# Optimization experiments

Measured on AMD Instinct MI355X. Metric: run time of the kernel, lower is better.

The kernel has to match this reference:

```python
import jax, jax.numpy as jnp
import numpy as np

COMMITMENT_COST = 0.25
NUM_EMBEDDINGS = 1024
EMBEDDING_DIM = 64


def setup_inputs() -> dict:
    key = jax.random.key(0)
    k1, k2 = jax.random.split(key)
    x = jax.random.normal(k1, (32, 64, 64, 64), dtype=jnp.float32)
    embeddings = jax.random.normal(k2, (EMBEDDING_DIM, NUM_EMBEDDINGS), dtype=jnp.float32)
    return {"x": x, "embeddings": embeddings}


def reference(x, embeddings):
    # x: [..., D], embeddings: [D, K]
    flat = jnp.reshape(x, (-1, EMBEDDING_DIM))                       # [N, D]
    # squared euclidean distances via ||a||^2 - 2 a.e + ||e||^2      # [N, K]
    distances = (jnp.sum(flat * flat, axis=1, keepdims=True)
                 - 2.0 * (flat @ embeddings)
                 + jnp.sum(embeddings * embeddings, axis=0, keepdims=True))
    flat_indices = jnp.argmax(-distances, axis=1)                    # [N]
    encodings = jax.nn.one_hot(flat_indices, NUM_EMBEDDINGS, dtype=distances.dtype)  # [N, K]
    encoding_indices = jnp.reshape(flat_indices, x.shape[:-1])
    # gather codebook rows: embeddings.T[idx]
    quantized = jnp.take(embeddings.T, encoding_indices, axis=0)     # same shape as x
    e_latent_loss = jnp.mean((jax.lax.stop_gradient(quantized) - x) ** 2)
    q_latent_loss = jnp.mean((quantized - jax.lax.stop_gradient(x)) ** 2)
    loss = q_latent_loss + COMMITMENT_COST * e_latent_loss
    quantized_st = x + jax.lax.stop_gradient(quantized - x)          # straight-through
    avg_probs = jnp.mean(encodings, axis=0)                          # [K]
    perplexity = jnp.exp(-jnp.sum(avg_probs * jnp.log(avg_probs + 1e-10)))
    return quantized_st, loss, perplexity, encodings, encoding_indices, distances
```

## Files before the change

kernel.cpp:

```cpp
#include <hip/hip_runtime.h>
#include <hip/hip_bf16.h>
#include <math.h>

#define NROWS 131072
#define DDIM  64
#define KCODE 1024
#define TAU_B 0.008f

#define OFF_Q    0L
#define OFF_LOSS 8388608L
#define OFF_PERP 8388609L
#define OFF_ENC  8388610L
#define OFF_IDX  (OFF_ENC + 134217728L)
#define OFF_DIST (OFF_IDX + 131072L)

#define WS_ENORM 0L
#define WS_ET    1024L
#define WS_EBPH  66560L
#define WS_EBPL  99328L
#define WS_CNT   263168L
#define WS_PART  395268L

typedef short bf16x8 __attribute__((ext_vector_type(8)));
typedef float f32x4  __attribute__((ext_vector_type(4)));
typedef float f32x2  __attribute__((ext_vector_type(2)));
typedef _Float16 f16x4v __attribute__((ext_vector_type(4)));

__device__ inline unsigned short f2bf(float f) {
    unsigned u = __float_as_uint(f);
    unsigned r = (u + 0x7fffu + ((u >> 16) & 1u)) >> 16;
    return (unsigned short)r;
}
__device__ inline float bf2f(unsigned short h) {
    return __uint_as_float(((unsigned)h) << 16);
}
__device__ inline int dswz16(int i) { return i ^ (((i >> 12) & 3) << 3); }

__global__ __launch_bounds__(256) void k1a_prep(const float* __restrict__ e,
                                                float* __restrict__ enorm,
                                                float* __restrict__ eT,
                                                int* __restrict__ cnt) {
    int k = blockIdx.x * 256 + threadIdx.x;
    float s = 0.f;
    #pragma unroll 8
    for (int d = 0; d < DDIM; ++d) {
        float v = e[(size_t)d * KCODE + k];
        s = fmaf(v, v, s);
        eT[(size_t)k * DDIM + d] = v;
    }
    enorm[k] = s;
    cnt[k] = 0;
}

__global__ __launch_bounds__(128) void k1b_pack(const float* __restrict__ e,
                                                unsigned short* __restrict__ ebph,
                                                unsigned short* __restrict__ ebpl) {
    const int gct = blockIdx.x;
    const int ks  = threadIdx.x >> 6;
    const int l   = threadIdx.x & 63;
    const int col = (gct << 4) | (l & 15);
    const int kb  = (ks << 5) + ((l >> 4) << 3);
    const size_t ob = ((size_t)((gct << 1) | ks) * 64 + l) * 8;
    #pragma unroll
    for (int j = 0; j < 8; ++j) {
        float f = e[(size_t)(kb + j) * KCODE + col];
        unsigned short h = f2bf(f);
        float lo = f - bf2f(h);
        ebph[ob + j] = h;
        ebpl[ob + j] = f2bf(lo);
    }
}

__global__ __launch_bounds__(256, 4) void kA_fused(const float* __restrict__ x,
                                                   const float* __restrict__ e,
                                                   const unsigned short* __restrict__ ebph,
                                                   const unsigned short* __restrict__ ebpl,
                                                   const float* __restrict__ enorm,
                                                   const float* __restrict__ eT,
                                                   float* __restrict__ dist,
                                                   float* __restrict__ enc,
                                                   float* __restrict__ outq,
                                                   float* __restrict__ outidx,
                                                   int* __restrict__ cnt,
                                                   float* __restrict__ partials) {
    __shared__ __align__(16) _Float16 dtH[16384];
    __shared__ float hd[2];
    __shared__ short xh[16 * 64];
    __shared__ short xl[16 * 64];
    __shared__ float xn[16];
    __shared__ float wm1[4][16], wm2[4][16];
    __shared__ int   wi1[4][16];
    __shared__ float ps[16];
    __shared__ int   sidx[16];
    __shared__ int   nearmask;
    __shared__ float xsh[DDIM];
    __shared__ double wbv[4];
    __shared__ int    wbi[4];

    const int tid  = threadIdx.x;
    const int lane = tid & 63;
    const int w    = tid >> 6;
    const int rowbase = blockIdx.x * 16;
    float* ebase = enc + ((size_t)blockIdx.x << 14);

    {
        if (tid == 0) nearmask = 0;
        float4 v = ((const float4*)(x + (size_t)rowbase * DDIM))[tid];
        int fi = tid * 4, r = fi >> 6, c = fi & 63;
        float fv[4] = {v.x, v.y, v.z, v.w};
        short hv[4], lv[4];
        #pragma unroll
        for (int q = 0; q < 4; ++q) {
            unsigned short hh = f2bf(fv[q]);
            hv[q] = (short)hh;
            lv[q] = (short)f2bf(fv[q] - bf2f(hh));
        }
        *(short4*)&xh[r * 64 + c] = make_short4(hv[0], hv[1], hv[2], hv[3]);
        *(short4*)&xl[r * 64 + c] = make_short4(lv[0], lv[1], lv[2], lv[3]);
        float s4 = fmaf(v.x, v.x, fmaf(v.y, v.y, fmaf(v.z, v.z, v.w * v.w)));
        #pragma unroll
        for (int m = 1; m < 16; m <<= 1) s4 += __shfl_xor(s4, m);
        if ((lane & 15) == 0) xn[r] = s4;
    }
    __syncthreads();

    const int arow = lane & 15, akb = (lane >> 4) << 3;
    bf16x8 ah0 = *(const bf16x8*)&xh[arow * 64 + akb];
    bf16x8 ah1 = *(const bf16x8*)&xh[arow * 64 + 32 + akb];
    bf16x8 al0 = *(const bf16x8*)&xl[arow * 64 + akb];
    bf16x8 al1 = *(const bf16x8*)&xl[arow * 64 + 32 + akb];

    const int wr   = (lane >> 4) << 2;
    const int colb = (w << 8) | (lane & 15);
    float xnv[4];
    #pragma unroll
    for (int r = 0; r < 4; ++r) xnv[r] = xn[wr + r];
    float env[16];
    #pragma unroll
    for (int ct = 0; ct < 16; ++ct) env[ct] = enorm[colb + (ct << 4)];

    float m1[4], m2[4];
    int   i1[4];
    #pragma unroll
    for (int r = 0; r < 4; ++r) { m1[r] = 3.4e38f; m2[r] = 3.4e38f; i1[r] = 1 << 30; }

    const f32x4 z4 = {0.f, 0.f, 0.f, 0.f};

    #pragma unroll 4
    for (int ct = 0; ct < 16; ++ct) {
        const int gct = (w << 4) | ct;
        const size_t bo = ((size_t)(gct << 1) * 64 + lane) * 8;
        bf16x8 bh0 = *(const bf16x8*)(ebph + bo);
        bf16x8 bh1 = *(const bf16x8*)(ebph + bo + 512);
        bf16x8 bl0 = *(const bf16x8*)(ebpl + bo);
        bf16x8 bl1 = *(const bf16x8*)(ebpl + bo + 512);

        {
            const int s = (ct << 8) + tid;
            if (s < 4095) {
                *(f32x4*)(ebase + 2 + (s << 2)) = z4;
            } else {
                *(f32x2*)(ebase)         = (f32x2){0.f, 0.f};
                *(f32x2*)(ebase + 16382) = (f32x2){0.f, 0.f};
            }
        }

        f32x4 d = {0.f, 0.f, 0.f, 0.f};
        d = __builtin_amdgcn_mfma_f32_16x16x32_bf16(ah0, bh0, d, 0, 0, 0);
        d = __builtin_amdgcn_mfma_f32_16x16x32_bf16(ah1, bh1, d, 0, 0, 0);
        d = __builtin_amdgcn_mfma_f32_16x16x32_bf16(ah0, bl0, d, 0, 0, 0);
        d = __builtin_amdgcn_mfma_f32_16x16x32_bf16(ah1, bl1, d, 0, 0, 0);
        d = __builtin_amdgcn_mfma_f32_16x16x32_bf16(al0, bh0, d, 0, 0, 0);
        d = __builtin_amdgcn_mfma_f32_16x16x32_bf16(al1, bh1, d, 0, 0, 0);

        const int col = colb + (ct << 4);
        #pragma unroll
        for (int r = 0; r < 4; ++r) {
            float o = fmaf(-2.f, d[r], xnv[r] + env[ct]);
            if (o < m1[r]) { m2[r] = m1[r]; m1[r] = o; i1[r] = col; }
            else if (o < m2[r]) m2[r] = o;
            const int fl = ((wr + r) << 10) + col;
            if (fl >= 2) dtH[dswz16(fl - 2)] = (_Float16)o;
            else         hd[fl] = o;
        }
    }

    #pragma unroll
    for (int m = 1; m < 16; m <<= 1) {
        #pragma unroll
        for (int r = 0; r < 4; ++r) {
            float om1 = __shfl_xor(m1[r], m);
            int   oi1 = __shfl_xor(i1[r], m);
            float om2 = __shfl_xor(m2[r], m);
            if (om1 < m1[r] || (om1 == m1[r] && oi1 < i1[r])) {
                m2[r] = fminf(m1[r], om2); m1[r] = om1; i1[r] = oi1;
            } else {
                m2[r] = fminf(m2[r], om1);
            }
        }
    }
    if ((lane & 15) == 0) {
        #pragma unroll
        for (int r = 0; r < 4; ++r) {
            wm1[w][wr + r] = m1[r];
            wm2[w][wr + r] = m2[r];
            wi1[w][wr + r] = i1[r];
        }
    }
    __syncthreads();
    if (tid < 16) {
        float bm1 = wm1[0][tid], bm2 = wm2[0][tid];
        int   bi  = wi1[0][tid];
        #pragma unroll
        for (int wv = 1; wv < 4; ++wv) {
            float om1 = wm1[wv][tid], om2 = wm2[wv][tid];
            int   oi  = wi1[wv][tid];
            if (om1 < bm1 || (om1 == bm1 && oi < bi)) {
                bm2 = fminf(bm1, om2); bm1 = om1; bi = oi;
            } else {
                bm2 = fminf(bm2, om1);
            }
        }
        sidx[tid] = bi;
        ps[tid]   = bm1;
        if (bm2 - bm1 < TAU_B) atomicOr(&nearmask, 1 << tid);
    }
    __syncthreads();

    {
        float* dbase = dist + ((size_t)rowbase << 10);
        #pragma unroll
        for (int j = 0; j < 16; ++j) {
            const int s = (j << 8) + tid;
            if (s < 4095) {
                const int i0 = s << 2;
                const int iw = dswz16(i0);
                f16x4v h = *(const f16x4v*)&dtH[iw];
                f32x4 v = {(float)h[0], (float)h[1], (float)h[2], (float)h[3]};
                *(f32x4*)(dbase + 2 + i0) = v;
            }
        }
        if (tid == 255) {
            const int it = dswz16(16380);
            *(f32x2*)(dbase)         = (f32x2){hd[0], hd[1]};
            *(f32x2*)(dbase + 16382) = (f32x2){(float)dtH[it], (float)dtH[it + 1]};
        }
    }

    if (nearmask) {
        for (int mrow = nearmask; mrow; mrow &= (mrow - 1)) {
            const int r = __ffs(mrow) - 1;
            if (tid < DDIM) xsh[tid] = x[(size_t)(rowbase + r) * DDIM + tid];
            __syncthreads();
            const int k0 = tid * 4;
            double dd[4] = {0.0, 0.0, 0.0, 0.0};
            for (int d = 0; d < DDIM; ++d) {
                double xd = (double)xsh[d];
                float4 ev = *(const float4*)(e + (size_t)d * KCODE + k0);
                double t0 = xd - (double)ev.x; dd[0] = fma(t0, t0, dd[0]);
                double t1 = xd - (double)ev.y; dd[1] = fma(t1, t1, dd[1]);
                double t2 = xd - (double)ev.z; dd[2] = fma(t2, t2, dd[2]);
                double t3 = xd - (double)ev.w; dd[3] = fma(t3, t3, dd[3]);
            }
            double best = dd[0]; int bidx = k0;
            #pragma unroll
            for (int c = 1; c < 4; ++c)
                if (dd[c] < best) { best = dd[c]; bidx = k0 + c; }
            #pragma unroll
            for (int m = 1; m < 64; m <<= 1) {
                double ob = __shfl_xor(best, m);
                int    oi = __shfl_xor(bidx, m);
                if (ob < best || (ob == best && oi < bidx)) { best = ob; bidx = oi; }
            }
            if (lane == 0) { wbv[w] = best; wbi[w] = bidx; }
            __syncthreads();
            if (tid == 0) {
                double bb = wbv[0]; int bi = wbi[0];
                #pragma unroll
                for (int wv = 1; wv < 4; ++wv)
                    if (wbv[wv] < bb || (wbv[wv] == bb && wbi[wv] < bi)) {
                        bb = wbv[wv]; bi = wbi[wv];
                    }
                sidx[r] = bi; ps[r] = (float)bb;
            }
            __syncthreads();
        }
    }

    if (tid < 16) {
        const int idx = sidx[tid];
        ebase[((size_t)tid << 10) + idx] = 1.0f;
        outidx[rowbase + tid] = (float)idx;
        atomicAdd(cnt + idx, 1);
    }
    {
        const int r = tid >> 4, c = tid & 15;
        const int idx = sidx[r];
        f32x4 ev = *(const f32x4*)(eT + (size_t)idx * DDIM + (c << 2));
        *((f32x4*)(outq + ((size_t)(rowbase + r) << 6)) + c) = ev;
    }
    if (tid == 64) {
        float s = 0.f;
        #pragma unroll
        for (int j = 0; j < 16; ++j) s += ps[j];
        partials[blockIdx.x] = s;
    }
}

__global__ __launch_bounds__(256) void k6_scalar(const float* __restrict__ partials,
                                                 const int* __restrict__ cnt,
                                                 float* __restrict__ outloss,
                                                 float* __restrict__ outperp) {
    __shared__ double sd[256];
    const int tid = threadIdx.x;
    double s = 0.0;
    for (int i = tid; i < 8192; i += 256) s += (double)partials[i];
    sd[tid] = s;
    __syncthreads();
    for (int st = 128; st > 0; st >>= 1) {
        if (tid < st) sd[tid] += sd[tid + st];
        __syncthreads();
    }
    const double total = sd[0];
    __syncthreads();
    double h = 0.0;
    for (int k = tid; k < KCODE; k += 256) {
        double p = (double)cnt[k] / (double)NROWS;
        h -= p * log(p + 1e-10);
    }
    sd[tid] = h;
    __syncthreads();
    for (int st = 128; st > 0; st >>= 1) {
        if (tid < st) sd[tid] += sd[tid + st];
        __syncthreads();
    }
    if (tid == 0) {
        *outloss = (float)(total * 1.25 / (double)((long)NROWS * DDIM));
        *outperp = (float)exp(sd[0]);
    }
}

extern "C" void kernel_launch(void* const* d_in, const int* in_sizes, int n_in,
                              void* d_out, int out_size, void* d_ws, size_t ws_size,
                              hipStream_t stream) {
    const float* x = (const float*)d_in[0];
    const float* e = (const float*)d_in[1];
    float* out = (float*)d_out;

    float* ws_f = (float*)d_ws;
    float* enorm   = ws_f + WS_ENORM;
    float* eT      = ws_f + WS_ET;
    unsigned short* ebph = (unsigned short*)(ws_f + WS_EBPH);
    unsigned short* ebpl = (unsigned short*)(ws_f + WS_EBPL);
    int*   cnt     = (int*)(ws_f + WS_CNT);
    float* partials= ws_f + WS_PART;

    float* outq    = out + OFF_Q;
    float* outloss = out + OFF_LOSS;
    float* outperp = out + OFF_PERP;
    float* enc     = out + OFF_ENC;
    float* outidx  = out + OFF_IDX;
    float* dist    = out + OFF_DIST;

    hipLaunchKernelGGL(k1a_prep, dim3(4),    dim3(256), 0, stream, e, enorm, eT, cnt);
    hipLaunchKernelGGL(k1b_pack, dim3(64),   dim3(128), 0, stream, e, ebph, ebpl);
    hipLaunchKernelGGL(kA_fused, dim3(8192), dim3(256), 0, stream, x, e, ebph, ebpl, enorm,
                       eT, dist, enc, outq, outidx, cnt, partials);
    hipLaunchKernelGGL(k6_scalar,dim3(1),    dim3(256), 0, stream, partials, cnt, outloss, outperp);
}
```

Before: 283.3 us.

## Make each wave own 16 rows over all codes, removing block-level barriers

Each wave now processes 16 rows across the full 1024-code codebook instead of splitting columns across four waves, so the cross-wave min reduction and __syncthreads barriers go away. Distances are staged in per-wave LDS in four 256-column chunks and streamed out right after each chunk, and the fp64 near-tie refinement runs per wave with 16 codes per lane. The grid shrinks to 2048 blocks of 64 rows. In exchange, each wave now reads the whole packed codebook and does a longer serial loop. The dist stores are only 8-byte aligned because of an offset of 2 floats.

```diff
diff --git a/kernel.cpp b/kernel.cpp
--- a/kernel.cpp
+++ b/kernel.cpp
@@ -25,6 +25,7 @@
 typedef float f32x4  __attribute__((ext_vector_type(4)));
 typedef float f32x2  __attribute__((ext_vector_type(2)));
 typedef _Float16 f16x4v __attribute__((ext_vector_type(4)));
+typedef float f32x4u __attribute__((ext_vector_type(4), aligned(8)));
 
 __device__ inline unsigned short f2bf(float f) {
     unsigned u = __float_as_uint(f);
@@ -34,7 +35,7 @@
 __device__ inline float bf2f(unsigned short h) {
     return __uint_as_float(((unsigned)h) << 16);
 }
-__device__ inline int dswz16(int i) { return i ^ (((i >> 12) & 3) << 3); }
+__device__ inline int cswz(int i) { return i ^ (((i >> 10) & 3) << 4); }
 
 __global__ __launch_bounds__(256) void k1a_prep(const float* __restrict__ e,
                                                 float* __restrict__ enorm,
@@ -71,58 +72,56 @@
     }
 }
 
-__global__ __launch_bounds__(256, 4) void kA_fused(const float* __restrict__ x,
-                                                   const float* __restrict__ e,
-                                                   const unsigned short* __restrict__ ebph,
-                                                   const unsigned short* __restrict__ ebpl,
-                                                   const float* __restrict__ enorm,
-                                                   const float* __restrict__ eT,
-                                                   float* __restrict__ dist,
-                                                   float* __restrict__ enc,
-                                                   float* __restrict__ outq,
-                                                   float* __restrict__ outidx,
-                                                   int* __restrict__ cnt,
-                                                   float* __restrict__ partials) {
-    __shared__ __align__(16) _Float16 dtH[16384];
-    __shared__ float hd[2];
-    __shared__ short xh[16 * 64];
-    __shared__ short xl[16 * 64];
-    __shared__ float xn[16];
-    __shared__ float wm1[4][16], wm2[4][16];
-    __shared__ int   wi1[4][16];
-    __shared__ float ps[16];
-    __shared__ int   sidx[16];
-    __shared__ int   nearmask;
-    __shared__ float xsh[DDIM];
-    __shared__ double wbv[4];
-    __shared__ int    wbi[4];
+__global__ __launch_bounds__(256, 4) void kA_dist(const float* __restrict__ x,
+                                                  const float* __restrict__ e,
+                                                  const unsigned short* __restrict__ ebph,
+                                                  const unsigned short* __restrict__ ebpl,
+                                                  const float* __restrict__ enorm,
+                                                  const float* __restrict__ eT,
+                                                  float* __restrict__ dist,
+                                                  float* __restrict__ enc,
+                                                  float* __restrict__ outq,
+                                                  float* __restrict__ outidx,
+                                                  int* __restrict__ cnt,
+                                                  float* __restrict__ partials) {
+    __shared__ __align__(16) _Float16 dtH[4][4096];
+    __shared__ float xnS[4][16];
+    __shared__ float psS[4][16];
+    __shared__ int   sidxS[4][16];
+    __shared__ int   flagsS[4];
 
     const int tid  = threadIdx.x;
     const int lane = tid & 63;
     const int w    = tid >> 6;
-    const int rowbase = blockIdx.x * 16;
-    float* ebase = enc + ((size_t)blockIdx.x << 14);
+    const int grow0 = blockIdx.x * 64 + w * 16;
+    float* encw = enc + ((size_t)grow0 << 10);
+    short* xh = (short*)&dtH[w][0];
+    short* xl = (short*)&dtH[w][1024];
+
+    if (lane == 0) flagsS[w] = 0;
 
     {
-        if (tid == 0) nearmask = 0;
-        float4 v = ((const float4*)(x + (size_t)rowbase * DDIM))[tid];
-        int fi = tid * 4, r = fi >> 6, c = fi & 63;
-        float fv[4] = {v.x, v.y, v.z, v.w};
-        short hv[4], lv[4];
+        const float* xrow = x + ((size_t)grow0 << 6);
         #pragma unroll
         for (int q = 0; q < 4; ++q) {
-            unsigned short hh = f2bf(fv[q]);
-            hv[q] = (short)hh;
-            lv[q] = (short)f2bf(fv[q] - bf2f(hh));
-        }
-        *(short4*)&xh[r * 64 + c] = make_short4(hv[0], hv[1], hv[2], hv[3]);
-        *(short4*)&xl[r * 64 + c] = make_short4(lv[0], lv[1], lv[2], lv[3]);
-        float s4 = fmaf(v.x, v.x, fmaf(v.y, v.y, fmaf(v.z, v.z, v.w * v.w)));
-        #pragma unroll
-        for (int m = 1; m < 16; m <<= 1) s4 += __shfl_xor(s4, m);
-        if ((lane & 15) == 0) xn[r] = s4;
-    }
-    __syncthreads();
+            float4 v = ((const float4*)xrow)[(q << 6) + lane];
+            const int row = (q << 2) + (lane >> 4), col = (lane & 15) << 2;
+            float fv[4] = {v.x, v.y, v.z, v.w};
+            short hv[4], lv[4];
+            #pragma unroll
+            for (int c = 0; c < 4; ++c) {
+                unsigned short hh = f2bf(fv[c]);
+                hv[c] = (short)hh;
+                lv[c] = (short)f2bf(fv[c] - bf2f(hh));
+            }
+            *(short4*)&xh[row * 64 + col] = make_short4(hv[0], hv[1], hv[2], hv[3]);
+            *(short4*)&xl[row * 64 + col] = make_short4(lv[0], lv[1], lv[2], lv[3]);
+            float s4 = fmaf(v.x, v.x, fmaf(v.y, v.y, fmaf(v.z, v.z, v.w * v.w)));
+            #pragma unroll
+            for (int m = 1; m < 16; m <<= 1) s4 += __shfl_xor(s4, m);
+            if ((lane & 15) == 0) xnS[w][row] = s4;
+        }
+    }
 
     const int arow = lane & 15, akb = (lane >> 4) << 3;
     bf16x8 ah0 = *(const bf16x8*)&xh[arow * 64 + akb];
@@ -130,14 +129,10 @@
     bf16x8 al0 = *(const bf16x8*)&xl[arow * 64 + akb];
     bf16x8 al1 = *(const bf16x8*)&xl[arow * 64 + 32 + akb];
 
-    const int wr   = (lane >> 4) << 2;
-    const int colb = (w << 8) | (lane & 15);
+    const int wr = (lane >> 4) << 2;
     float xnv[4];
     #pragma unroll
-    for (int r = 0; r < 4; ++r) xnv[r] = xn[wr + r];
-    float env[16];
-    #pragma unroll
-    for (int ct = 0; ct < 16; ++ct) env[ct] = enorm[colb + (ct << 4)];
+    for (int r = 0; r < 4; ++r) xnv[r] = xnS[w][wr + r];
 
     float m1[4], m2[4];
     int   i1[4];
@@ -146,42 +141,50 @@
 
     const f32x4 z4 = {0.f, 0.f, 0.f, 0.f};
 
-    #pragma unroll 4
-    for (int ct = 0; ct < 16; ++ct) {
-        const int gct = (w << 4) | ct;
-        const size_t bo = ((size_t)(gct << 1) * 64 + lane) * 8;
-        bf16x8 bh0 = *(const bf16x8*)(ebph + bo);
-        bf16x8 bh1 = *(const bf16x8*)(ebph + bo + 512);
-        bf16x8 bl0 = *(const bf16x8*)(ebpl + bo);
-        bf16x8 bl1 = *(const bf16x8*)(ebpl + bo + 512);
-
-        {
-            const int s = (ct << 8) + tid;
-            if (s < 4095) {
-                *(f32x4*)(ebase + 2 + (s << 2)) = z4;
-            } else {
-                *(f32x2*)(ebase)         = (f32x2){0.f, 0.f};
-                *(f32x2*)(ebase + 16382) = (f32x2){0.f, 0.f};
-            }
-        }
-
-        f32x4 d = {0.f, 0.f, 0.f, 0.f};
-        d = __builtin_amdgcn_mfma_f32_16x16x32_bf16(ah0, bh0, d, 0, 0, 0);
-        d = __builtin_amdgcn_mfma_f32_16x16x32_bf16(ah1, bh1, d, 0, 0, 0);
-        d = __builtin_amdgcn_mfma_f32_16x16x32_bf16(ah0, bl0, d, 0, 0, 0);
-        d = __builtin_amdgcn_mfma_f32_16x16x32_bf16(ah1, bl1, d, 0, 0, 0);
-        d = __builtin_amdgcn_mfma_f32_16x16x32_bf16(al0, bh0, d, 0, 0, 0);
-        d = __builtin_amdgcn_mfma_f32_16x16x32_bf16(al1, bh1, d, 0, 0, 0);
-
-        const int col = colb + (ct << 4);
-        #pragma unroll
-        for (int r = 0; r < 4; ++r) {
-            float o = fmaf(-2.f, d[r], xnv[r] + env[ct]);
-            if (o < m1[r]) { m2[r] = m1[r]; m1[r] = o; i1[r] = col; }
-            else if (o < m2[r]) m2[r] = o;
-            const int fl = ((wr + r) << 10) + col;
-            if (fl >= 2) dtH[dswz16(fl - 2)] = (_Float16)o;
-            else         hd[fl] = o;
+    for (int ch = 0; ch < 4; ++ch) {
+        #pragma unroll 4
+        for (int cc = 0; cc < 16; ++cc) {
+            const int ct = (ch << 4) | cc;
+            const size_t bo = ((size_t)(ct << 1) * 64 + lane) * 8;
+            bf16x8 bh0 = *(const bf16x8*)(ebph + bo);
+            bf16x8 bh1 = *(const bf16x8*)(ebph + bo + 512);
+            bf16x8 bl0 = *(const bf16x8*)(ebpl + bo);
+            bf16x8 bl1 = *(const bf16x8*)(ebpl + bo + 512);
+
+            {
+                const int s = (ct << 6) + lane;
+                if (s < 4095) {
+                    *(f32x4*)(encw + 2 + (s << 2)) = z4;
+                } else {
+                    *(f32x2*)(encw)         = (f32x2){0.f, 0.f};
+                    *(f32x2*)(encw + 16382) = (f32x2){0.f, 0.f};
+                }
+            }
+            const float env = enorm[(ct << 4) + (lane & 15)];
+
+            f32x4 d = {0.f, 0.f, 0.f, 0.f};
+            d = __builtin_amdgcn_mfma_f32_16x16x32_bf16(ah0, bh0, d, 0, 0, 0);
+            d = __builtin_amdgcn_mfma_f32_16x16x32_bf16(ah1, bh1, d, 0, 0, 0);
+            d = __builtin_amdgcn_mfma_f32_16x16x32_bf16(ah0, bl0, d, 0, 0, 0);
+            d = __builtin_amdgcn_mfma_f32_16x16x32_bf16(ah1, bl1, d, 0, 0, 0);
+            d = __builtin_amdgcn_mfma_f32_16x16x32_bf16(al0, bh0, d, 0, 0, 0);
+            d = __builtin_amdgcn_mfma_f32_16x16x32_bf16(al1, bh1, d, 0, 0, 0);
+
+            const int col = (ct << 4) | (lane & 15);
+            #pragma unroll
+            for (int r = 0; r < 4; ++r) {
+                float o = fmaf(-2.f, d[r], xnv[r] + env);
+                if (o < m1[r]) { m2[r] = m1[r]; m1[r] = o; i1[r] = col; }
+                else if (o < m2[r]) m2[r] = o;
+                const int fl = ((wr + r) << 8) + (cc << 4) + (lane & 15);
+                dtH[w][cswz(fl)] = (_Float16)o;
+            }
+        }
+        #pragma unroll
+        for (int r = 0; r < 16; ++r) {
+            f16x4v h = *(const f16x4v*)&dtH[w][cswz((r << 8) + (lane << 2))];
+            f32x4u v = {(float)h[0], (float)h[1], (float)h[2], (float)h[3]};
+            *(f32x4u*)(dist + ((size_t)(grow0 + r) << 10) + (ch << 8) + (lane << 2)) = v;
         }
     }
 
@@ -200,110 +203,71 @@
         }
     }
     if ((lane & 15) == 0) {
+        int nib = 0;
         #pragma unroll
         for (int r = 0; r < 4; ++r) {
-            wm1[w][wr + r] = m1[r];
-            wm2[w][wr + r] = m2[r];
-            wi1[w][wr + r] = i1[r];
-        }
-    }
-    __syncthreads();
-    if (tid < 16) {
-        float bm1 = wm1[0][tid], bm2 = wm2[0][tid];
-        int   bi  = wi1[0][tid];
-        #pragma unroll
-        for (int wv = 1; wv < 4; ++wv) {
-            float om1 = wm1[wv][tid], om2 = wm2[wv][tid];
-            int   oi  = wi1[wv][tid];
-            if (om1 < bm1 || (om1 == bm1 && oi < bi)) {
-                bm2 = fminf(bm1, om2); bm1 = om1; bi = oi;
-            } else {
-                bm2 = fminf(bm2, om1);
-            }
-        }
-        sidx[tid] = bi;
-        ps[tid]   = bm1;
-        if (bm2 - bm1 < TAU_B) atomicOr(&nearmask, 1 << tid);
-    }
-    __syncthreads();
-
-    {
-        float* dbase = dist + ((size_t)rowbase << 10);
-        #pragma unroll
-        for (int j = 0; j < 16; ++j) {
-            const int s = (j << 8) + tid;
-            if (s < 4095) {
-                const int i0 = s << 2;
-                const int iw = dswz16(i0);
-                f16x4v h = *(const f16x4v*)&dtH[iw];
-                f32x4 v = {(float)h[0], (float)h[1], (float)h[2], (float)h[3]};
-                *(f32x4*)(dbase + 2 + i0) = v;
-            }
-        }
-        if (tid == 255) {
-            const int it = dswz16(16380);
-            *(f32x2*)(dbase)         = (f32x2){hd[0], hd[1]};
-            *(f32x2*)(dbase + 16382) = (f32x2){(float)dtH[it], (float)dtH[it + 1]};
-        }
-    }
-
-    if (nearmask) {
-        for (int mrow = nearmask; mrow; mrow &= (mrow - 1)) {
-            const int r = __ffs(mrow) - 1;
-            if (tid < DDIM) xsh[tid] = x[(size_t)(rowbase + r) * DDIM + tid];
-            __syncthreads();
-            const int k0 = tid * 4;
-            double dd[4] = {0.0, 0.0, 0.0, 0.0};
-            for (int d = 0; d < DDIM; ++d) {
-                double xd = (double)xsh[d];
-                float4 ev = *(const float4*)(e + (size_t)d * KCODE + k0);
-                double t0 = xd - (double)ev.x; dd[0] = fma(t0, t0, dd[0]);
-                double t1 = xd - (double)ev.y; dd[1] = fma(t1, t1, dd[1]);
-                double t2 = xd - (double)ev.z; dd[2] = fma(t2, t2, dd[2]);
-                double t3 = xd - (double)ev.w; dd[3] = fma(t3, t3, dd[3]);
-            }
-            double best = dd[0]; int bidx = k0;
+            sidxS[w][wr + r] = i1[r];
+            psS[w][wr + r]   = m1[r];
+            if (m2[r] - m1[r] < TAU_B) nib |= 1 << r;
+        }
+        if (nib) atomicOr(&flagsS[w], nib << wr);
+    }
+
+    int fmask = flagsS[w];
+    while (fmask) {
+        const int r = __ffs(fmask) - 1;
+        fmask &= fmask - 1;
+        const float xv = x[((size_t)(grow0 + r) << 6) + lane];
+        double dd[16];
+        #pragma unroll
+        for (int kk = 0; kk < 16; ++kk) dd[kk] = 0.0;
+        for (int di = 0; di < DDIM; ++di) {
+            const double xd = (double)__shfl(xv, di);
+            const float* ep = e + ((size_t)di << 10) + (lane << 4);
             #pragma unroll
-            for (int c = 1; c < 4; ++c)
-                if (dd[c] < best) { best = dd[c]; bidx = k0 + c; }
-            #pragma unroll
-            for (int m = 1; m < 64; m <<= 1) {
-                double ob = __shfl_xor(best, m);
-                int    oi = __shfl_xor(bidx, m);
-                if (ob < best || (ob == best && oi < bidx)) { best = ob; bidx = oi; }
-            }
-            if (lane == 0) { wbv[w] = best; wbi[w] = bidx; }
-            __syncthreads();
-            if (tid == 0) {
-                double bb = wbv[0]; int bi = wbi[0];
+            for (int g = 0; g < 4; ++g) {
+                f32x4 ev = *(const f32x4*)(ep + (g << 2));
                 #pragma unroll
-                for (int wv = 1; wv < 4; ++wv)
-                    if (wbv[wv] < bb || (wbv[wv] == bb && wbi[wv] < bi)) {
-                        bb = wbv[wv]; bi = wbi[wv];
-                    }
-                sidx[r] = bi; ps[r] = (float)bb;
-            }
-            __syncthreads();
-        }
-    }
-
-    if (tid < 16) {
-        const int idx = sidx[tid];
-        ebase[((size_t)tid << 10) + idx] = 1.0f;
-        outidx[rowbase + tid] = (float)idx;
+                for (int c = 0; c < 4; ++c) {
+                    double t = xd - (double)ev[c];
+                    dd[(g << 2) + c] = fma(t, t, dd[(g << 2) + c]);
+                }
+            }
+        }
+        double best = dd[0];
+        int bidx = lane << 4;
+        #pragma unroll
+        for (int kk = 1; kk < 16; ++kk)
+            if (dd[kk] < best) { best = dd[kk]; bidx = (lane << 4) + kk; }
+        #pragma unroll
+        for (int m = 1; m < 64; m <<= 1) {
+            double ob = __shfl_xor(best, m);
+            int    oi = __shfl_xor(bidx, m);
+            if (ob < best || (ob == best && oi < bidx)) { best = ob; bidx = oi; }
+        }
+        if (lane == 0) { sidxS[w][r] = bidx; psS[w][r] = (float)best; }
+    }
+
+    __builtin_amdgcn_s_waitcnt(0x3f70);
+
+    if (lane < 16) {
+        const int idx = sidxS[w][lane];
+        encw[((size_t)lane << 10) + idx] = 1.0f;
+        outidx[grow0 + lane] = (float)idx;
         atomicAdd(cnt + idx, 1);
     }
-    {
-        const int r = tid >> 4, c = tid & 15;
-        const int idx = sidx[r];
-        f32x4 ev = *(const f32x4*)(eT + (size_t)idx * DDIM + (c << 2));
-        *((f32x4*)(outq + ((size_t)(rowbase + r) << 6)) + c) = ev;
-    }
-    if (tid == 64) {
+    #pragma unroll
+    for (int q = 0; q < 4; ++q) {
+        const int r = (q << 2) + (lane >> 4);
+        const int idx = sidxS[w][r];
+        f32x4 ev = *(const f32x4*)(eT + ((size_t)idx << 6) + ((lane & 15) << 2));
+        *((f32x4*)(outq + ((size_t)(grow0 + r) << 6)) + (lane & 15)) = ev;
+    }
+    if (lane == 0) {
         float s = 0.f;
         #pragma unroll
-        for (int j = 0; j < 16; ++j) s += ps[j];
-        partials[blockIdx.x] = s;
+        for (int j = 0; j < 16; ++j) s += psS[w][j];
+        partials[(blockIdx.x << 2) + w] = s;
     }
 }
 
@@ -364,7 +328,7 @@
 
     hipLaunchKernelGGL(k1a_prep, dim3(4),    dim3(256), 0, stream, e, enorm, eT, cnt);
     hipLaunchKernelGGL(k1b_pack, dim3(64),   dim3(128), 0, stream, e, ebph, ebpl);
-    hipLaunchKernelGGL(kA_fused, dim3(8192), dim3(256), 0, stream, x, e, ebph, ebpl, enorm,
+    hipLaunchKernelGGL(kA_dist,  dim3(2048), dim3(256), 0, stream, x, e, ebph, ebpl, enorm,
                        eT, dist, enc, outq, outidx, cnt, partials);
     hipLaunchKernelGGL(k6_scalar,dim3(1),    dim3(256), 0, stream, partials, cnt, outloss, outperp);
 }
```

Measured after the change: 522.4 us. 1.84x slower.

## Interleave codebook column tiles across waves and overlap distance writeback with compute

Applied to the files above, without the earlier changes.

Codebook column tiles are reassigned so all four waves finish the first half of the 1024 columns (512 per row) together. After a barrier, the second compute half streams the already-finished half of the distance tile out of LDS to global memory alongside the MFMA work. The rest is written after a second barrier, so the fp32 distance store overlaps compute instead of following it. The cost is an extra block barrier and more complex index and edge handling for the unaligned offset-2 layout.

```diff
diff --git a/kernel.cpp b/kernel.cpp
--- a/kernel.cpp
+++ b/kernel.cpp
@@ -25,6 +25,7 @@
 typedef float f32x4  __attribute__((ext_vector_type(4)));
 typedef float f32x2  __attribute__((ext_vector_type(2)));
 typedef _Float16 f16x4v __attribute__((ext_vector_type(4)));
+typedef _Float16 f16x2v __attribute__((ext_vector_type(2)));
 
 __device__ inline unsigned short f2bf(float f) {
     unsigned u = __float_as_uint(f);
@@ -35,6 +36,12 @@
     return __uint_as_float(((unsigned)h) << 16);
 }
 __device__ inline int dswz16(int i) { return i ^ (((i >> 12) & 3) << 3); }
+
+__device__ inline void lds_barrier() {
+    asm volatile("s_waitcnt lgkmcnt(0)" ::: "memory");
+    __builtin_amdgcn_s_barrier();
+    __builtin_amdgcn_sched_barrier(0);
+}
 
 __global__ __launch_bounds__(256) void k1a_prep(const float* __restrict__ e,
                                                 float* __restrict__ enorm,
@@ -101,7 +108,8 @@
     const int lane = tid & 63;
     const int w    = tid >> 6;
     const int rowbase = blockIdx.x * 16;
-    float* ebase = enc + ((size_t)blockIdx.x << 14);
+    float* encw  = enc  + ((size_t)blockIdx.x << 14);
+    float* dbase = dist + ((size_t)rowbase << 10);
 
     {
         if (tid == 0) nearmask = 0;
@@ -130,14 +138,14 @@
     bf16x8 al0 = *(const bf16x8*)&xl[arow * 64 + akb];
     bf16x8 al1 = *(const bf16x8*)&xl[arow * 64 + 32 + akb];
 
-    const int wr   = (lane >> 4) << 2;
-    const int colb = (w << 8) | (lane & 15);
+    const int wr = (lane >> 4) << 2;
     float xnv[4];
     #pragma unroll
     for (int r = 0; r < 4; ++r) xnv[r] = xn[wr + r];
     float env[16];
     #pragma unroll
-    for (int ct = 0; ct < 16; ++ct) env[ct] = enorm[colb + (ct << 4)];
+    for (int c = 0; c < 16; ++c)
+        env[c] = enorm[(((c << 2) | w) << 4) + (lane & 15)];
 
     float m1[4], m2[4];
     int   i1[4];
@@ -147,23 +155,21 @@
     const f32x4 z4 = {0.f, 0.f, 0.f, 0.f};
 
     #pragma unroll 4
-    for (int ct = 0; ct < 16; ++ct) {
-        const int gct = (w << 4) | ct;
+    for (int c = 0; c < 8; ++c) {
+        const int gct = (c << 2) | w;
+        {
+            const int s = (c << 8) + tid;
+            if (s < 4095) *(f32x4*)(encw + 2 + (s << 2)) = z4;
+            else {
+                *(f32x2*)(encw)         = (f32x2){0.f, 0.f};
+                *(f32x2*)(encw + 16382) = (f32x2){0.f, 0.f};
+            }
+        }
         const size_t bo = ((size_t)(gct << 1) * 64 + lane) * 8;
         bf16x8 bh0 = *(const bf16x8*)(ebph + bo);
         bf16x8 bh1 = *(const bf16x8*)(ebph + bo + 512);
         bf16x8 bl0 = *(const bf16x8*)(ebpl + bo);
         bf16x8 bl1 = *(const bf16x8*)(ebpl + bo + 512);
-
-        {
-            const int s = (ct << 8) + tid;
-            if (s < 4095) {
-                *(f32x4*)(ebase + 2 + (s << 2)) = z4;
-            } else {
-                *(f32x2*)(ebase)         = (f32x2){0.f, 0.f};
-                *(f32x2*)(ebase + 16382) = (f32x2){0.f, 0.f};
-            }
-        }
 
         f32x4 d = {0.f, 0.f, 0.f, 0.f};
         d = __builtin_amdgcn_mfma_f32_16x16x32_bf16(ah0, bh0, d, 0, 0, 0);
@@ -173,15 +179,73 @@
         d = __builtin_amdgcn_mfma_f32_16x16x32_bf16(al0, bh0, d, 0, 0, 0);
         d = __builtin_amdgcn_mfma_f32_16x16x32_bf16(al1, bh1, d, 0, 0, 0);
 
-        const int col = colb + (ct << 4);
+        const int col = (gct << 4) | (lane & 15);
         #pragma unroll
         for (int r = 0; r < 4; ++r) {
-            float o = fmaf(-2.f, d[r], xnv[r] + env[ct]);
+            float o = fmaf(-2.f, d[r], xnv[r] + env[c]);
             if (o < m1[r]) { m2[r] = m1[r]; m1[r] = o; i1[r] = col; }
             else if (o < m2[r]) m2[r] = o;
             const int fl = ((wr + r) << 10) + col;
             if (fl >= 2) dtH[dswz16(fl - 2)] = (_Float16)o;
             else         hd[fl] = o;
+        }
+    }
+
+    lds_barrier();
+
+    #pragma unroll 4
+    for (int c = 8; c < 16; ++c) {
+        const int gct = (c << 2) | w;
+        {
+            const int s = (c << 8) + tid;
+            if (s < 4095) *(f32x4*)(encw + 2 + (s << 2)) = z4;
+            else {
+                *(f32x2*)(encw)         = (f32x2){0.f, 0.f};
+                *(f32x2*)(encw + 16382) = (f32x2){0.f, 0.f};
+            }
+        }
+        {
+            const int f = ((c - 8) << 8) + tid;
+            const int row = f >> 7, k = f & 127;
+            if (k < 127) {
+                const int j0 = (row << 10) + (k << 2);
+                f16x4v h = *(const f16x4v*)&dtH[dswz16(j0)];
+                *(f32x4*)(dbase + 2 + j0) =
+                    (f32x4){(float)h[0], (float)h[1], (float)h[2], (float)h[3]};
+            } else {
+                float h0, h1;
+                if (row == 0) { h0 = hd[0]; h1 = hd[1]; }
+                else {
+                    f16x2v t = *(const f16x2v*)&dtH[dswz16((row << 10) - 2)];
+                    h0 = (float)t[0]; h1 = (float)t[1];
+                }
+                *(f32x2*)(dbase + (row << 10)) = (f32x2){h0, h1};
+                f16x2v t2 = *(const f16x2v*)&dtH[dswz16((row << 10) + 508)];
+                *(f32x2*)(dbase + (row << 10) + 510) = (f32x2){(float)t2[0], (float)t2[1]};
+            }
+        }
+        const size_t bo = ((size_t)(gct << 1) * 64 + lane) * 8;
+        bf16x8 bh0 = *(const bf16x8*)(ebph + bo);
+        bf16x8 bh1 = *(const bf16x8*)(ebph + bo + 512);
+        bf16x8 bl0 = *(const bf16x8*)(ebpl + bo);
+        bf16x8 bl1 = *(const bf16x8*)(ebpl + bo + 512);
+
+        f32x4 d = {0.f, 0.f, 0.f, 0.f};
+        d = __builtin_amdgcn_mfma_f32_16x16x32_bf16(ah0, bh0, d, 0, 0, 0);
+        d = __builtin_amdgcn_mfma_f32_16x16x32_bf16(ah1, bh1, d, 0, 0, 0);
+        d = __builtin_amdgcn_mfma_f32_16x16x32_bf16(ah0, bl0, d, 0, 0, 0);
+        d = __builtin_amdgcn_mfma_f32_16x16x32_bf16(ah1, bl1, d, 0, 0, 0);
+        d = __builtin_amdgcn_mfma_f32_16x16x32_bf16(al0, bh0, d, 0, 0, 0);
+        d = __builtin_amdgcn_mfma_f32_16x16x32_bf16(al1, bh1, d, 0, 0, 0);
+
+        const int col = (gct << 4) | (lane & 15);
+        #pragma unroll
+        for (int r = 0; r < 4; ++r) {
+            float o = fmaf(-2.f, d[r], xnv[r] + env[c]);
+            if (o < m1[r]) { m2[r] = m1[r]; m1[r] = o; i1[r] = col; }
+            else if (o < m2[r]) m2[r] = o;
+            const int fl = ((wr + r) << 10) + col;
+            dtH[dswz16(fl - 2)] = (_Float16)o;
         }
     }
 
@@ -207,7 +271,26 @@
             wi1[w][wr + r] = i1[r];
         }
     }
-    __syncthreads();
+
+    lds_barrier();
+
+    #pragma unroll
+    for (int it = 0; it < 8; ++it) {
+        const int f = (it << 8) + tid;
+        const int row = f >> 7, k = f & 127;
+        if (k < 127) {
+            const int j0 = (row << 10) + 512 + (k << 2);
+            f16x4v h = *(const f16x4v*)&dtH[dswz16(j0)];
+            *(f32x4*)(dbase + 2 + j0) =
+                (f32x4){(float)h[0], (float)h[1], (float)h[2], (float)h[3]};
+        } else {
+            f16x2v th = *(const f16x2v*)&dtH[dswz16((row << 10) + 510)];
+            *(f32x2*)(dbase + (row << 10) + 512) = (f32x2){(float)th[0], (float)th[1]};
+            f16x2v tt = *(const f16x2v*)&dtH[dswz16((row << 10) + 1020)];
+            *(f32x2*)(dbase + (row << 10) + 1022) = (f32x2){(float)tt[0], (float)tt[1]};
+        }
+    }
+
     if (tid < 16) {
         float bm1 = wm1[0][tid], bm2 = wm2[0][tid];
         int   bi  = wi1[0][tid];
@@ -226,26 +309,6 @@
         if (bm2 - bm1 < TAU_B) atomicOr(&nearmask, 1 << tid);
     }
     __syncthreads();
-
-    {
-        float* dbase = dist + ((size_t)rowbase << 10);
-        #pragma unroll
-        for (int j = 0; j < 16; ++j) {
-            const int s = (j << 8) + tid;
-            if (s < 4095) {
-                const int i0 = s << 2;
-                const int iw = dswz16(i0);
-                f16x4v h = *(const f16x4v*)&dtH[iw];
-                f32x4 v = {(float)h[0], (float)h[1], (float)h[2], (float)h[3]};
-                *(f32x4*)(dbase + 2 + i0) = v;
-            }
-        }
-        if (tid == 255) {
-            const int it = dswz16(16380);
-            *(f32x2*)(dbase)         = (f32x2){hd[0], hd[1]};
-            *(f32x2*)(dbase + 16382) = (f32x2){(float)dtH[it], (float)dtH[it + 1]};
-        }
-    }
 
     if (nearmask) {
         for (int mrow = nearmask; mrow; mrow &= (mrow - 1)) {
@@ -289,7 +352,7 @@
 
     if (tid < 16) {
         const int idx = sidx[tid];
-        ebase[((size_t)tid << 10) + idx] = 1.0f;
+        encw[((size_t)tid << 10) + idx] = 1.0f;
         outidx[rowbase + tid] = (float)idx;
         atomicAdd(cnt + idx, 1);
     }
```

Result: slower. 320.4 us (+13.1%).
